# Kernel optimization log

Measured on AMD Instinct MI355X. Metric: run time of the kernel, lower is better.

The kernel has to match this reference:

```python
import jax, jax.numpy as jnp
import numpy as np

B, N, C = 4, 4096, 64
ALPHA = 0.2        # leaky relu slope
THRESHOLD = 0.5    # adjacency threshold
NEG_INF = -9e15


def setup_inputs() -> dict:
    key = jax.random.key(0)
    k1, k2, k3 = jax.random.split(key, 3)
    inp = jax.random.normal(k1, (B, N, C), dtype=jnp.float32)
    adj = jax.random.uniform(k2, (N, N), dtype=jnp.float32)
    # xavier_uniform with gain=1.414 on shape (2C, 1)
    bound = 1.414 * float(np.sqrt(6.0 / (2 * C + 1)))
    a = jax.random.uniform(k3, (2 * C, 1), dtype=jnp.float32, minval=-bound, maxval=bound)
    return {"input": inp, "adj": adj, "a": a}


def reference(input, adj, a):
    h = input                          # [B, N, C]
    a1 = a[:C, 0]                      # scores from source node i
    a2 = a[C:, 0]                      # scores from target node j
    # e[b,i,j] = leakyrelu(a1.h_i + a2.h_j)  (avoids O(N^2 * 2C) concat)
    s1 = h @ a1                        # [B, N]
    s2 = h @ a2                        # [B, N]
    e = s1[:, :, None] + s2[:, None, :]
    e = jnp.where(e > 0, e, ALPHA * e)
    mask = adj[None, :, :] > THRESHOLD
    att = jnp.where(mask, e, NEG_INF)
    att = jax.nn.softmax(att, axis=2)  # [B, N, N]
    h_prime = jnp.einsum('bij,bjc->bic', att, h)
    return jax.nn.elu(h_prime)         # concat=True -> elu
```

## Files before the change

### kernel.cpp

```cpp
#include <hip/hip_runtime.h>
#include <hip/hip_bf16.h>

#define B_ 4
#define N_ 4096
#define C_ 64

constexpr float LOG2E = 1.44269504088896340736f;

typedef __attribute__((ext_vector_type(8))) short short8;
typedef __attribute__((ext_vector_type(4))) float f32x4;

#if __has_builtin(__builtin_amdgcn_exp2f)
#define EXP2F(x) __builtin_amdgcn_exp2f(x)
#else
#define EXP2F(x) exp2f(x)
#endif

static __device__ inline short f32_to_bf16_bits(float f) {
    union { __hip_bfloat16 h; unsigned short u; } cv;
    cv.h = __float2bfloat16(f);
    return (short)cv.u;
}

__global__ __launch_bounds__(256) void gat_prep_s(
    const float* __restrict__ h, const float* __restrict__ a,
    float* __restrict__ s1s, float* __restrict__ s2s)
{
    const int wave = threadIdx.x >> 6;
    const int lane = threadIdx.x & 63;
    const int row = blockIdx.x * 4 + wave;
    float hv = h[(size_t)row * C_ + lane];
    float p1 = hv * a[lane];
    float p2 = hv * a[C_ + lane];
#pragma unroll
    for (int o = 32; o >= 1; o >>= 1) {
        p1 += __shfl_xor(p1, o, 64);
        p2 += __shfl_xor(p2, o, 64);
    }
    if (lane == 0) {
        s1s[row] = p1 * LOG2E;
        s2s[row] = p2 * LOG2E;
    }
}

__global__ __launch_bounds__(256) void gat_prep_t(
    const float* __restrict__ h, unsigned short* __restrict__ hT)
{
    const int bid = blockIdx.x;
    const int b = bid >> 6;
    const int i0 = (bid & 63) * 64;
    __shared__ float tile[64][65];
    const int t = threadIdx.x;
    {
        const int rr = t >> 2;
        const int cc = (t & 3) * 16;
        const float* src = h + ((size_t)(b * N_ + i0 + rr)) * C_ + cc;
#pragma unroll
        for (int k = 0; k < 16; k += 4) {
            float4 v = *(const float4*)(src + k);
            tile[rr][cc + k + 0] = v.x;
            tile[rr][cc + k + 1] = v.y;
            tile[rr][cc + k + 2] = v.z;
            tile[rr][cc + k + 3] = v.w;
        }
    }
    __syncthreads();
    {
        const int c  = t >> 2;
        const int ic = (t & 3) * 16;
        short8 w0, w1;
#pragma unroll
        for (int k = 0; k < 8; ++k)
            w0[k] = f32_to_bf16_bits(tile[ic + k][c]);
#pragma unroll
        for (int k = 0; k < 8; ++k)
            w1[k] = f32_to_bf16_bits(tile[ic + 8 + k][c]);
        unsigned short* dst = hT + ((size_t)(b * C_ + c)) * N_ + i0 + ic;
        *(short8*)(dst)     = w0;
        *(short8*)(dst + 8) = w1;
    }
}

__global__ __launch_bounds__(256) void gat_main(
    const float* __restrict__ adj, const float* __restrict__ s1s,
    const float* __restrict__ s2s, const unsigned short* __restrict__ hT,
    float* __restrict__ accP, float* __restrict__ lP, int jsNum)
{
    const int bid  = blockIdx.x;
    const int itb  = bid / jsNum;
    const int js   = bid % jsNum;
    const int jlen = N_ / jsNum;
    const int j0   = js * jlen;
    const int i0   = itb * 64;
    const int wave = threadIdx.x >> 6;
    const int lane = threadIdx.x & 63;
    const int b    = wave;
    const int g    = lane >> 4;
    const int r16  = lane & 15;

    float s1v[4];
#pragma unroll
    for (int it = 0; it < 4; ++it)
        s1v[it] = s1s[b * N_ + i0 + it * 16 + r16];

    f32x4 acc[4][4];
#pragma unroll
    for (int it = 0; it < 4; ++it)
#pragma unroll
        for (int ct = 0; ct < 4; ++ct)
            acc[it][ct] = (f32x4){0.f, 0.f, 0.f, 0.f};
    float lpart[4] = {0.f, 0.f, 0.f, 0.f};

    const unsigned short* hTb = hT + (size_t)b * C_ * N_;
    const float* s2b = s2s + b * N_;

    for (int jj = 0; jj < jlen; jj += 32) {
        const int kb = j0 + jj + g * 8;

        short8 bfrag[4];
#pragma unroll
        for (int ct = 0; ct < 4; ++ct)
            bfrag[ct] = *(const short8*)(hTb + (size_t)(ct * 16 + r16) * N_ + kb);

        float4 s2a = *(const float4*)(s2b + kb);
        float4 s2c = *(const float4*)(s2b + kb + 4);
        float s2v[8] = {s2a.x, s2a.y, s2a.z, s2a.w, s2c.x, s2c.y, s2c.z, s2c.w};

#pragma unroll
        for (int it = 0; it < 4; ++it) {
            const float* arow = adj + (size_t)(i0 + it * 16 + r16) * N_ + kb;
            float4 a0 = *(const float4*)(arow);
            float4 a1 = *(const float4*)(arow + 4);
            float adjv[8] = {a0.x, a0.y, a0.z, a0.w, a1.x, a1.y, a1.z, a1.w};

            const float s1 = s1v[it];
            short8 afrag;
#pragma unroll
            for (int q = 0; q < 8; ++q) {
                float e = s1 + s2v[q];
                e = fmaxf(e, 0.2f * e);
                float p = (adjv[q] > 0.5f) ? EXP2F(e) : 0.0f;
                lpart[it] += p;
                afrag[q] = f32_to_bf16_bits(p);
            }
#pragma unroll
            for (int ct = 0; ct < 4; ++ct)
                acc[it][ct] = __builtin_amdgcn_mfma_f32_16x16x32_bf16(
                    afrag, bfrag[ct], acc[it][ct], 0, 0, 0);
        }
    }

#pragma unroll
    for (int it = 0; it < 4; ++it) {
        float v = lpart[it];
        v += __shfl_xor(v, 16, 64);
        v += __shfl_xor(v, 32, 64);
        lpart[it] = v;
    }

    const size_t pb = (size_t)js * B_ + b;
    if (g == 0) {
#pragma unroll
        for (int it = 0; it < 4; ++it)
            lP[pb * N_ + i0 + it * 16 + r16] = lpart[it];
    }

    float* accBase = accP + pb * (size_t)N_ * C_;
#pragma unroll
    for (int it = 0; it < 4; ++it)
#pragma unroll
        for (int ct = 0; ct < 4; ++ct)
#pragma unroll
            for (int r = 0; r < 4; ++r) {
                const int i = i0 + it * 16 + g * 4 + r;
                const int c = ct * 16 + r16;
                accBase[(size_t)i * C_ + c] = acc[it][ct][r];
            }
}

__global__ __launch_bounds__(256) void gat_combine(
    const float* __restrict__ accP, const float* __restrict__ lP,
    float* __restrict__ out, int jsNum)
{
    const int t = blockIdx.x * 256 + threadIdx.x;
    if (t >= B_ * N_ * C_) return;
    const int bi = t / C_;
    float asum = 0.f, lsum = 0.f;
    for (int p = 0; p < jsNum; ++p) {
        asum += accP[(size_t)p * (B_ * N_ * C_) + t];
        lsum += lP[(size_t)p * (B_ * N_) + bi];
    }
    const float x = asum / lsum;
    out[t] = (x > 0.f) ? x : (expf(x) - 1.f);
}

extern "C" void kernel_launch(void* const* d_in, const int* in_sizes, int n_in,
                              void* d_out, int out_size, void* d_ws, size_t ws_size,
                              hipStream_t stream)
{
    const float* h   = (const float*)d_in[0];
    const float* adj = (const float*)d_in[1];
    const float* a   = (const float*)d_in[2];
    float* out = (float*)d_out;

    char* ws = (char*)d_ws;
    float* s1s = (float*)ws;
    float* s2s = (float*)(ws + (size_t)B_ * N_ * 4);
    unsigned short* hT = (unsigned short*)(ws + (size_t)2 * B_ * N_ * 4);
    const size_t lOff = (size_t)2 * B_ * N_ * 4 + (size_t)B_ * C_ * N_ * 2;

    int jsNum = 8;
    while (jsNum > 1) {
        size_t need = lOff + (size_t)jsNum * B_ * N_ * 4
                           + (size_t)jsNum * B_ * N_ * C_ * 4;
        if (need <= ws_size) break;
        jsNum >>= 1;
    }
    float* lP   = (float*)(ws + lOff);
    float* accP = (float*)(ws + lOff + (size_t)jsNum * B_ * N_ * 4);

    gat_prep_s<<<B_ * N_ / 4, 256, 0, stream>>>(h, a, s1s, s2s);
    gat_prep_t<<<B_ * (N_ / 64), 256, 0, stream>>>(h, hT);
    gat_main<<<64 * jsNum, 256, 0, stream>>>(adj, s1s, s2s, hT, accP, lP, jsNum);
    gat_combine<<<(B_ * N_ * C_ + 255) / 256, 256, 0, stream>>>(accP, lP, out, jsNum);
}
```

Before: 154.6 us.

## Fuse prep kernels, halve main row tile, double-buffer loads, vectorize combine

Merges the score-dot-product and bf16 transpose prep kernels into one launch. The main kernel now covers 32 rows per block instead of 64, which doubles the grid and reduces accumulator registers; it also adds launch bounds for occupancy. Global loads for the next 32-column tile are issued before computing the current one, in a register double-buffer, to hide memory latency. The combine kernel is vectorized to float4 and uses a reciprocal multiply. The cost is that each block reads hT twice as often relative to its adj reads, and register pressure from holding two tiles.

```diff
diff --git a/kernel.cpp b/kernel.cpp
--- a/kernel.cpp
+++ b/kernel.cpp
@@ -22,29 +22,10 @@
     return (short)cv.u;
 }
 
-__global__ __launch_bounds__(256) void gat_prep_s(
+__global__ __launch_bounds__(256) void gat_prep(
     const float* __restrict__ h, const float* __restrict__ a,
-    float* __restrict__ s1s, float* __restrict__ s2s)
-{
-    const int wave = threadIdx.x >> 6;
-    const int lane = threadIdx.x & 63;
-    const int row = blockIdx.x * 4 + wave;
-    float hv = h[(size_t)row * C_ + lane];
-    float p1 = hv * a[lane];
-    float p2 = hv * a[C_ + lane];
-#pragma unroll
-    for (int o = 32; o >= 1; o >>= 1) {
-        p1 += __shfl_xor(p1, o, 64);
-        p2 += __shfl_xor(p2, o, 64);
-    }
-    if (lane == 0) {
-        s1s[row] = p1 * LOG2E;
-        s2s[row] = p2 * LOG2E;
-    }
-}
-
-__global__ __launch_bounds__(256) void gat_prep_t(
-    const float* __restrict__ h, unsigned short* __restrict__ hT)
+    float* __restrict__ s1s, float* __restrict__ s2s,
+    unsigned short* __restrict__ hT)
 {
     const int bid = blockIdx.x;
     const int b = bid >> 6;
@@ -55,6 +36,7 @@
         const int rr = t >> 2;
         const int cc = (t & 3) * 16;
         const float* src = h + ((size_t)(b * N_ + i0 + rr)) * C_ + cc;
+        float d1 = 0.f, d2 = 0.f;
 #pragma unroll
         for (int k = 0; k < 16; k += 4) {
             float4 v = *(const float4*)(src + k);
@@ -62,6 +44,16 @@
             tile[rr][cc + k + 1] = v.y;
             tile[rr][cc + k + 2] = v.z;
             tile[rr][cc + k + 3] = v.w;
+            float4 a1 = *(const float4*)(a + cc + k);
+            float4 a2 = *(const float4*)(a + C_ + cc + k);
+            d1 += v.x * a1.x + v.y * a1.y + v.z * a1.z + v.w * a1.w;
+            d2 += v.x * a2.x + v.y * a2.y + v.z * a2.z + v.w * a2.w;
+        }
+        d1 += __shfl_xor(d1, 1, 64); d1 += __shfl_xor(d1, 2, 64);
+        d2 += __shfl_xor(d2, 1, 64); d2 += __shfl_xor(d2, 2, 64);
+        if ((t & 3) == 0) {
+            s1s[b * N_ + i0 + rr] = d1 * LOG2E;
+            s2s[b * N_ + i0 + rr] = d2 * LOG2E;
         }
     }
     __syncthreads();
@@ -81,7 +73,58 @@
     }
 }
 
-__global__ __launch_bounds__(256) void gat_main(
+struct JTile {
+    short8 bfrag[4];
+    float  s2v[8];
+    float  adjv[2][8];
+};
+
+static __device__ inline void load_tile(
+    JTile& T, const unsigned short* __restrict__ hTb,
+    const float* __restrict__ s2b,
+    const float* __restrict__ adjR0, const float* __restrict__ adjR1,
+    int kb, int r16)
+{
+#pragma unroll
+    for (int ct = 0; ct < 4; ++ct)
+        T.bfrag[ct] = *(const short8*)(hTb + (size_t)(ct * 16 + r16) * N_ + kb);
+    float4 sa = *(const float4*)(s2b + kb);
+    float4 sb = *(const float4*)(s2b + kb + 4);
+    T.s2v[0] = sa.x; T.s2v[1] = sa.y; T.s2v[2] = sa.z; T.s2v[3] = sa.w;
+    T.s2v[4] = sb.x; T.s2v[5] = sb.y; T.s2v[6] = sb.z; T.s2v[7] = sb.w;
+    float4 a0 = *(const float4*)(adjR0 + kb);
+    float4 a1 = *(const float4*)(adjR0 + kb + 4);
+    T.adjv[0][0] = a0.x; T.adjv[0][1] = a0.y; T.adjv[0][2] = a0.z; T.adjv[0][3] = a0.w;
+    T.adjv[0][4] = a1.x; T.adjv[0][5] = a1.y; T.adjv[0][6] = a1.z; T.adjv[0][7] = a1.w;
+    float4 b0 = *(const float4*)(adjR1 + kb);
+    float4 b1 = *(const float4*)(adjR1 + kb + 4);
+    T.adjv[1][0] = b0.x; T.adjv[1][1] = b0.y; T.adjv[1][2] = b0.z; T.adjv[1][3] = b0.w;
+    T.adjv[1][4] = b1.x; T.adjv[1][5] = b1.y; T.adjv[1][6] = b1.z; T.adjv[1][7] = b1.w;
+}
+
+static __device__ inline void compute_tile(
+    const JTile& T, const float* s1v, f32x4 acc[2][4], float* lpart)
+{
+#pragma unroll
+    for (int it = 0; it < 2; ++it) {
+        short8 afrag;
+        const float s1 = s1v[it];
+#pragma unroll
+        for (int q = 0; q < 8; ++q) {
+            float e = s1 + T.s2v[q];
+            e = fmaxf(e, 0.2f * e);
+            float p = (T.adjv[it][q] > 0.5f) ? EXP2F(e) : 0.0f;
+            lpart[it] += p;
+            afrag[q] = f32_to_bf16_bits(p);
+        }
+#pragma unroll
+        for (int ct = 0; ct < 4; ++ct)
+            acc[it][ct] = __builtin_amdgcn_mfma_f32_16x16x32_bf16(
+                afrag, T.bfrag[ct], acc[it][ct], 0, 0, 0);
+    }
+}
+
+__global__ __launch_bounds__(256, 4) void gat_main(
     const float* __restrict__ adj, const float* __restrict__ s1s,
     const float* __restrict__ s2s, const unsigned short* __restrict__ hT,
     float* __restrict__ accP, float* __restrict__ lP, int jsNum)
@@ -91,67 +134,42 @@
     const int js   = bid % jsNum;
     const int jlen = N_ / jsNum;
     const int j0   = js * jlen;
-    const int i0   = itb * 64;
-    const int wave = threadIdx.x >> 6;
+    const int i0   = itb * 32;
     const int lane = threadIdx.x & 63;
-    const int b    = wave;
+    const int b    = threadIdx.x >> 6;
     const int g    = lane >> 4;
     const int r16  = lane & 15;
 
-    float s1v[4];
-#pragma unroll
-    for (int it = 0; it < 4; ++it)
-        s1v[it] = s1s[b * N_ + i0 + it * 16 + r16];
-
-    f32x4 acc[4][4];
-#pragma unroll
-    for (int it = 0; it < 4; ++it)
+    float s1v[2];
+    s1v[0] = s1s[b * N_ + i0 + r16];
+    s1v[1] = s1s[b * N_ + i0 + 16 + r16];
+
+    f32x4 acc[2][4];
+#pragma unroll
+    for (int it = 0; it < 2; ++it)
 #pragma unroll
         for (int ct = 0; ct < 4; ++ct)
             acc[it][ct] = (f32x4){0.f, 0.f, 0.f, 0.f};
-    float lpart[4] = {0.f, 0.f, 0.f, 0.f};
+    float lpart[2] = {0.f, 0.f};
 
     const unsigned short* hTb = hT + (size_t)b * C_ * N_;
-    const float* s2b = s2s + b * N_;
-
-    for (int jj = 0; jj < jlen; jj += 32) {
-        const int kb = j0 + jj + g * 8;
-
-        short8 bfrag[4];
-#pragma unroll
-        for (int ct = 0; ct < 4; ++ct)
-            bfrag[ct] = *(const short8*)(hTb + (size_t)(ct * 16 + r16) * N_ + kb);
-
-        float4 s2a = *(const float4*)(s2b + kb);
-        float4 s2c = *(const float4*)(s2b + kb + 4);
-        float s2v[8] = {s2a.x, s2a.y, s2a.z, s2a.w, s2c.x, s2c.y, s2c.z, s2c.w};
-
-#pragma unroll
-        for (int it = 0; it < 4; ++it) {
-            const float* arow = adj + (size_t)(i0 + it * 16 + r16) * N_ + kb;
-            float4 a0 = *(const float4*)(arow);
-            float4 a1 = *(const float4*)(arow + 4);
-            float adjv[8] = {a0.x, a0.y, a0.z, a0.w, a1.x, a1.y, a1.z, a1.w};
-
-            const float s1 = s1v[it];
-            short8 afrag;
-#pragma unroll
-            for (int q = 0; q < 8; ++q) {
-                float e = s1 + s2v[q];
-                e = fmaxf(e, 0.2f * e);
-                float p = (adjv[q] > 0.5f) ? EXP2F(e) : 0.0f;
-                lpart[it] += p;
-                afrag[q] = f32_to_bf16_bits(p);
-            }
-#pragma unroll
-            for (int ct = 0; ct < 4; ++ct)
-                acc[it][ct] = __builtin_amdgcn_mfma_f32_16x16x32_bf16(
-                    afrag, bfrag[ct], acc[it][ct], 0, 0, 0);
-        }
-    }
-
-#pragma unroll
-    for (int it = 0; it < 4; ++it) {
+    const float* s2b   = s2s + b * N_;
+    const float* adjR0 = adj + (size_t)(i0 + r16) * N_;
+    const float* adjR1 = adj + (size_t)(i0 + 16 + r16) * N_;
+    const int kbase = j0 + g * 8;
+
+    JTile tA, tB;
+    load_tile(tA, hTb, s2b, adjR0, adjR1, kbase, r16);
+    for (int base = 0; base + 64 <= jlen; base += 64) {
+        load_tile(tB, hTb, s2b, adjR0, adjR1, kbase + base + 32, r16);
+        compute_tile(tA, s1v, acc, lpart);
+        if (base + 64 < jlen)
+            load_tile(tA, hTb, s2b, adjR0, adjR1, kbase + base + 64, r16);
+        compute_tile(tB, s1v, acc, lpart);
+    }
+
+#pragma unroll
+    for (int it = 0; it < 2; ++it) {
         float v = lpart[it];
         v += __shfl_xor(v, 16, 64);
         v += __shfl_xor(v, 32, 64);
@@ -160,14 +178,13 @@
 
     const size_t pb = (size_t)js * B_ + b;
     if (g == 0) {
-#pragma unroll
-        for (int it = 0; it < 4; ++it)
-            lP[pb * N_ + i0 + it * 16 + r16] = lpart[it];
+        lP[pb * N_ + i0 + r16]      = lpart[0];
+        lP[pb * N_ + i0 + 16 + r16] = lpart[1];
     }
 
     float* accBase = accP + pb * (size_t)N_ * C_;
 #pragma unroll
-    for (int it = 0; it < 4; ++it)
+    for (int it = 0; it < 2; ++it)
 #pragma unroll
         for (int ct = 0; ct < 4; ++ct)
 #pragma unroll
@@ -183,15 +200,24 @@
     float* __restrict__ out, int jsNum)
 {
     const int t = blockIdx.x * 256 + threadIdx.x;
-    if (t >= B_ * N_ * C_) return;
-    const int bi = t / C_;
-    float asum = 0.f, lsum = 0.f;
+    const int total4 = B_ * N_ * C_ / 4;
+    if (t >= total4) return;
+    const int bi = t >> 4;
+    float4 asum = {0.f, 0.f, 0.f, 0.f};
+    float lsum = 0.f;
     for (int p = 0; p < jsNum; ++p) {
-        asum += accP[(size_t)p * (B_ * N_ * C_) + t];
+        float4 v = ((const float4*)accP)[(size_t)p * total4 + t];
+        asum.x += v.x; asum.y += v.y; asum.z += v.z; asum.w += v.w;
         lsum += lP[(size_t)p * (B_ * N_) + bi];
     }
-    const float x = asum / lsum;
-    out[t] = (x > 0.f) ? x : (expf(x) - 1.f);
+    const float inv = 1.0f / lsum;
+    float4 o;
+    o.x = asum.x * inv; o.y = asum.y * inv; o.z = asum.z * inv; o.w = asum.w * inv;
+    o.x = (o.x > 0.f) ? o.x : (expf(o.x) - 1.f);
+    o.y = (o.y > 0.f) ? o.y : (expf(o.y) - 1.f);
+    o.z = (o.z > 0.f) ? o.z : (expf(o.z) - 1.f);
+    o.w = (o.w > 0.f) ? o.w : (expf(o.w) - 1.f);
+    ((float4*)out)[t] = o;
 }
 
 extern "C" void kernel_launch(void* const* d_in, const int* in_sizes, int n_in,
@@ -219,8 +245,7 @@
     float* lP   = (float*)(ws + lOff);
     float* accP = (float*)(ws + lOff + (size_t)jsNum * B_ * N_ * 4);
 
-    gat_prep_s<<<B_ * N_ / 4, 256, 0, stream>>>(h, a, s1s, s2s);
-    gat_prep_t<<<B_ * (N_ / 64), 256, 0, stream>>>(h, hT);
-    gat_main<<<64 * jsNum, 256, 0, stream>>>(adj, s1s, s2s, hT, accP, lP, jsNum);
-    gat_combine<<<(B_ * N_ * C_ + 255) / 256, 256, 0, stream>>>(accP, lP, out, jsNum);
-}
+    gat_prep<<<B_ * (N_ / 64), 256, 0, stream>>>(h, a, s1s, s2s, hT);
+    gat_main<<<128 * jsNum, 256, 0, stream>>>(adj, s1s, s2s, hT, accP, lP, jsNum);
+    gat_combine<<<(B_ * N_ * C_ / 4 + 255) / 256, 256, 0, stream>>>(accP, lP, out, jsNum);
+}
```

After: 220.2 us. 1.42x slower.
